# Kernel tuning notes

Measured on AMD Instinct MI355X. Metric: run time of the kernel, lower is better.

Reference implementation:

```python
import jax, jax.numpy as jnp
import numpy as np

STRIDES = [8, 16, 32]
INPUT = 640
NC = 80
NA = 3
B = 16
NGT = 32
LS = 0.0
BOX_W = 0.05 * 3.0
OBJ_W = 1.0 * 5.0
CLS_W = 0.5
NOOBJ_W = 0.5
IOU_THR = 0.5
EPS = 1e-7


def _bce(x, t):
    # BCEWithLogits, elementwise, numerically stable
    return jnp.maximum(x, 0.0) - x * t + jnp.log1p(jnp.exp(-jnp.abs(x)))


def _iou_gt_anchor(gt, anch):
    # gt: [..., 4] xyxy; anch: [..., 4] (cx, cy, w, h)
    ax1 = anch[..., 0] - anch[..., 2] * 0.5
    ay1 = anch[..., 1] - anch[..., 3] * 0.5
    ax2 = anch[..., 0] + anch[..., 2] * 0.5
    ay2 = anch[..., 1] + anch[..., 3] * 0.5
    iw = jnp.clip(jnp.minimum(gt[..., 2], ax2) - jnp.maximum(gt[..., 0], ax1), 0.0)
    ih = jnp.clip(jnp.minimum(gt[..., 3], ay2) - jnp.maximum(gt[..., 1], ay1), 0.0)
    inter = iw * ih
    a_gt = (gt[..., 2] - gt[..., 0]) * (gt[..., 3] - gt[..., 1])
    a_an = anch[..., 2] * anch[..., 3]
    return inter / (a_gt + a_an - inter + EPS)


def _assign_one(gt_boxes, gt_labels, anchors, stride):
    # Vectorized version of the per-box Python assignment loop.
    # gt_boxes: [N,4] xyxy; anchors: [A,H,W,4] cxcywh
    A, H, W, _ = anchors.shape
    N = gt_boxes.shape[0]
    gcx = (gt_boxes[:, 0] + gt_boxes[:, 2]) * 0.5
    gcy = (gt_boxes[:, 1] + gt_boxes[:, 3]) * 0.5
    gx = jnp.clip((gcx / stride).astype(jnp.int32), 0, W - 1)
    gy = jnp.clip((gcy / stride).astype(jnp.int32), 0, H - 1)
    cell = anchors[:, gy, gx, :]                      # [A, N, 4]
    iou = _iou_gt_anchor(gt_boxes[None, :, :], cell)  # [A, N]
    pos = iou > IOU_THR
    has = pos.any(axis=0)                             # [N]
    fb = jnp.arange(A)[:, None] == jnp.argmax(iou, axis=0)[None, :]
    pos = jnp.where(has[None, :], pos, fb)            # argmax fallback
    flat = gy * W + gx                                # [N]
    key = jnp.arange(A)[:, None] * (H * W) + flat[None, :]  # [A, N]
    cand = jnp.where(pos, iou, -1.0)
    best = jnp.full(A * H * W, -1.0, jnp.float32).at[key.ravel()].max(cand.ravel())
    gtid = jnp.broadcast_to(jnp.arange(N, dtype=jnp.int32)[None, :], (A, N))
    isb = pos & (cand >= best[key])
    win = jnp.full(A * H * W, N, jnp.int32).at[key.ravel()].min(
        jnp.where(isb, gtid, N).ravel().astype(jnp.int32))
    mask = win < N                                    # [A*H*W]
    wid = jnp.minimum(win, N - 1)
    obj_t = mask.astype(jnp.float32).reshape(A, H, W)
    oh = jax.nn.one_hot(gt_labels[wid], NC, dtype=jnp.float32)
    if LS > 0:
        oh = oh * (1.0 - LS) + LS / NC
    cls_t = (oh * mask[:, None].astype(jnp.float32)).reshape(A, H, W, NC)
    gt_cell = gt_boxes[wid].reshape(A, H, W, 4)
    return obj_t, cls_t, gt_cell


def _decode(box_pred, anchors, stride):
    # YOLOv5-style decode (assumed; _decode_boxes not in source snippet)
    s = jax.nn.sigmoid(box_pred)
    cx = anchors[..., 0] + (s[..., 0] * 2.0 - 0.5) * stride
    cy = anchors[..., 1] + (s[..., 1] * 2.0 - 0.5) * stride
    w = anchors[..., 2] * (s[..., 2] * 2.0) ** 2
    h = anchors[..., 3] * (s[..., 3] * 2.0) ** 2
    return jnp.stack([cx - w * 0.5, cy - h * 0.5, cx + w * 0.5, cy + h * 0.5], axis=-1)


def _ciou(b1, b2):
    # both xyxy, same shape; standard CIoU with detached alpha
    w1 = b1[..., 2] - b1[..., 0]; h1 = b1[..., 3] - b1[..., 1]
    w2 = b2[..., 2] - b2[..., 0]; h2 = b2[..., 3] - b2[..., 1]
    iw = jnp.clip(jnp.minimum(b1[..., 2], b2[..., 2]) - jnp.maximum(b1[..., 0], b2[..., 0]), 0.0)
    ih = jnp.clip(jnp.minimum(b1[..., 3], b2[..., 3]) - jnp.maximum(b1[..., 1], b2[..., 1]), 0.0)
    inter = iw * ih
    union = w1 * h1 + w2 * h2 - inter + EPS
    iou = inter / union
    cw = jnp.maximum(b1[..., 2], b2[..., 2]) - jnp.minimum(b1[..., 0], b2[..., 0])
    ch = jnp.maximum(b1[..., 3], b2[..., 3]) - jnp.minimum(b1[..., 1], b2[..., 1])
    c2 = cw ** 2 + ch ** 2 + EPS
    rho2 = ((b2[..., 0] + b2[..., 2] - b1[..., 0] - b1[..., 2]) ** 2 +
            (b2[..., 1] + b2[..., 3] - b1[..., 1] - b1[..., 3]) ** 2) * 0.25
    v = (4.0 / (jnp.pi ** 2)) * (jnp.arctan(w2 / (h2 + EPS)) - jnp.arctan(w1 / (h1 + EPS))) ** 2
    alpha = jax.lax.stop_gradient(v / (v - iou + (1.0 + EPS)))
    return iou - rho2 / c2 - alpha * v


def _scale_loss(pred, anch, gt_boxes, gt_labels, stride):
    box_pred = pred[..., :4]
    obj_pred = pred[..., 4]
    cls_pred = pred[..., 5:]
    obj_t, cls_t, gt_cell = jax.vmap(
        lambda b, l: _assign_one(b, l, anch, stride))(gt_boxes, gt_labels)
    pred_boxes = _decode(box_pred, anch, stride)           # [B,A,H,W,4]
    ciou = _ciou(pred_boxes, gt_cell)                       # [B,A,H,W]
    pos = obj_t > 0
    valid = pos & jnp.isfinite(ciou)
    n_valid = valid.sum()
    box_loss = jnp.where(valid, 1.0 - ciou, 0.0).sum() / jnp.maximum(n_valid, 1)
    wgt = jnp.where(pos, 1.0, NOOBJ_W)
    obj_loss = (_bce(obj_pred, obj_t) * wgt).sum() / (wgt.sum() + 1e-6)
    n_pos = pos.sum()
    cls_loss = (_bce(cls_pred, cls_t) * obj_t[..., None]).sum() / jnp.maximum(n_pos * NC, 1)
    return box_loss, obj_loss, cls_loss, n_valid


def _total(p0, p1, p2, a0, a1, a2, gt_boxes, gt_labels):
    bl = ol = cl = jnp.float32(0.0)
    tv = jnp.int32(0)
    for pred, anch, s in zip((p0, p1, p2), (a0, a1, a2), STRIDES):
        b, o, c, nv = _scale_loss(pred, anch, gt_boxes, gt_labels, float(s))
        bl = bl + b; ol = ol + o; cl = cl + c; tv = tv + nv
    ns = 3.0
    bl = jnp.where(tv > 0, bl / ns, bl)
    cl = jnp.where(tv > 0, cl / ns, cl)
    ol = ol / ns
    total = BOX_W * bl + OBJ_W * ol + CLS_W * cl
    return jnp.where(jnp.isfinite(total), total, 0.0)


def _make_anchors():
    wh = np.array([[[10, 13], [16, 30], [33, 23]],
                   [[30, 61], [62, 45], [59, 119]],
                   [[116, 90], [156, 198], [373, 326]]], np.float32)
    out = []
    for si, s in enumerate(STRIDES):
        H = W = INPUT // s
        yy, xx = np.meshgrid(np.arange(H), np.arange(W), indexing='ij')
        a = np.zeros((NA, H, W, 4), np.float32)
        a[..., 0] = ((xx + 0.5) * s).astype(np.float32)
        a[..., 1] = ((yy + 0.5) * s).astype(np.float32)
        a[..., 2] = wh[si, :, 0][:, None, None]
        a[..., 3] = wh[si, :, 1][:, None, None]
        out.append(jnp.asarray(a))
    return out


def setup_inputs() -> dict:
    key = jax.random.key(0)
    ks = jax.random.split(key, 6)
    p0 = jax.random.normal(ks[0], (B, NA, 80, 80, 5 + NC), jnp.float32)
    p1 = jax.random.normal(ks[1], (B, NA, 40, 40, 5 + NC), jnp.float32)
    p2 = jax.random.normal(ks[2], (B, NA, 20, 20, 5 + NC), jnp.float32)
    a0, a1, a2 = _make_anchors()
    cxy = jax.random.uniform(ks[3], (B, NGT, 2), jnp.float32, 32.0, INPUT - 32.0)
    wh = jax.random.uniform(ks[4], (B, NGT, 2), jnp.float32, 16.0, 256.0)
    x1y1 = jnp.clip(cxy - wh * 0.5, 0.0, float(INPUT))
    x2y2 = jnp.clip(cxy + wh * 0.5, 0.0, float(INPUT))
    gt_boxes = jnp.concatenate([x1y1, x2y2], axis=-1)
    gt_labels = jax.random.randint(ks[5], (B, NGT), 0, NC, jnp.int32)
    return {"p0": p0, "p1": p1, "p2": p2, "a0": a0, "a1": a1, "a2": a2,
            "gt_boxes": gt_boxes, "gt_labels": gt_labels}


def reference(p0, p1, p2, a0, a1, a2, gt_boxes, gt_labels):
    return _total(p0, p1, p2, a0, a1, a2, gt_boxes, gt_labels)
```

## Files before the change

kernel.cpp:

```cpp
#include <hip/hip_runtime.h>
#include <math.h>

#define NC 80
#define NA 3
#define BATCH 16
#define NGT 32
#define IOU_THR 0.5f
#define FEPS 1e-7f

#define ASSIGN_GRID 48
#define OBJ_BLOCKS 168
#define POS_BLOCKS 288
#define LOSS_GRID (OBJ_BLOCKS + POS_BLOCKS)

#define A_SLOT(a)  (128 * (a))
#define OBJ_SLOT(j) (6144 + 32 * (j))
#define POS_SLOT(j) (11520 + 32 * (j))

__device__ __forceinline__ float bce_f(float x, float t) {
    return fmaxf(x, 0.f) - x * t + log1pf(expf(-fabsf(x)));
}

__global__ __launch_bounds__(128) void assign_kernel(
    const float* __restrict__ gt_boxes,
    const float* __restrict__ a0, const float* __restrict__ a1, const float* __restrict__ a2,
    int* ws_i)
{
    const int bid = blockIdx.x;
    const int si = bid % 3;
    const int b  = bid / 3;
    const int W  = 80 >> si;
    const int HW = W * W;
    const float s = (float)(8 << si);
    const float* anch = (si == 0) ? a0 : (si == 1) ? a1 : a2;

    __shared__ float gtb[NGT][4];
    __shared__ int   gflat[NGT];
    __shared__ float giou[NA][NGT];
    __shared__ float gcand[NA][NGT];
    __shared__ unsigned char gpos[NA][NGT];
    __shared__ unsigned char gisb[NA][NGT];
    __shared__ int wlist[NA * NGT];
    __shared__ int wcnt2[2];
    __shared__ int s_wn;

    const int t = threadIdx.x;
    const int lane = t & 63, wv = t >> 6;
    gtb[t >> 2][t & 3] = gt_boxes[b * NGT * 4 + t];
    __syncthreads();

    if (t < NGT) {
        float x1 = gtb[t][0], y1 = gtb[t][1], x2 = gtb[t][2], y2 = gtb[t][3];
        float gcx = (x1 + x2) * 0.5f, gcy = (y1 + y2) * 0.5f;
        int gx = (int)(gcx / s); gx = min(max(gx, 0), W - 1);
        int gy = (int)(gcy / s); gy = min(max(gy, 0), W - 1);
        gflat[t] = gy * W + gx;
    }
    __syncthreads();

    if (t < NA * NGT) {
        int a = t >> 5, n = t & 31;
        int flat = gflat[n];
        const float* ap = anch + ((size_t)a * HW + flat) * 4;
        float acx = ap[0], acy = ap[1], aw = ap[2], ah = ap[3];
        float ax1 = acx - aw * 0.5f, ay1 = acy - ah * 0.5f;
        float ax2 = acx + aw * 0.5f, ay2 = acy + ah * 0.5f;
        float x1 = gtb[n][0], y1 = gtb[n][1], x2 = gtb[n][2], y2 = gtb[n][3];
        float iw = fmaxf(fminf(x2, ax2) - fmaxf(x1, ax1), 0.f);
        float ih = fmaxf(fminf(y2, ay2) - fmaxf(y1, ay1), 0.f);
        float inter = iw * ih;
        float a_gt = (x2 - x1) * (y2 - y1);
        float a_an = aw * ah;
        giou[a][n] = inter / (a_gt + a_an - inter + FEPS);
    }
    __syncthreads();

    if (t < NA * NGT) {
        int a = t >> 5, n = t & 31;
        float i0 = giou[0][n], i1 = giou[1][n], i2 = giou[2][n];
        bool has = (i0 > IOU_THR) || (i1 > IOU_THR) || (i2 > IOU_THR);
        int amax = 0; float bv = i0;
        if (i1 > bv) { bv = i1; amax = 1; }
        if (i2 > bv) { bv = i2; amax = 2; }
        float iou = giou[a][n];
        bool ps = has ? (iou > IOU_THR) : (a == amax);
        gpos[a][n] = ps ? 1 : 0;
        gcand[a][n] = ps ? iou : -1.0f;
    }
    __syncthreads();

    if (t < NA * NGT) {
        int a = t >> 5, n = t & 31;
        int flat = gflat[n];
        float best = -1.0f;
        for (int m = 0; m < NGT; ++m)
            if (gflat[m] == flat) best = fmaxf(best, gcand[a][m]);
        gisb[a][n] = (gpos[a][n] && gcand[a][n] >= best) ? 1 : 0;
    }
    __syncthreads();

    int win = 0, pack = 0;
    if (t < NA * NGT) {
        int a = t >> 5, n = t & 31;
        if (gisb[a][n]) {
            int flat = gflat[n];
            bool first = true;
            for (int m = 0; m < n; ++m)
                if (gflat[m] == flat && gisb[a][m]) { first = false; break; }
            if (first) { win = 1; pack = flat | (a << 13) | (n << 19); }
        }
    }
    unsigned long long mask = __ballot(win);
    if (lane == 0) wcnt2[wv] = (int)__popcll(mask);
    __syncthreads();
    if (win) {
        int base = wv ? wcnt2[0] : 0;
        int idx = base + (int)__popcll(mask & ((1ull << lane) - 1ull));
        wlist[idx] = pack;
    }
    if (t == 0) s_wn = wcnt2[0] + wcnt2[1];
    __syncthreads();
    const int wn = s_wn;

    int* slot = ws_i + A_SLOT(bid);
    if (t == 0) slot[0] = wn;
    if (t < 96) slot[1 + t] = (t < wn) ? wlist[t] : 0;
}

__global__ __launch_bounds__(256) void loss_kernel(
    const float* __restrict__ p0, const float* __restrict__ p1, const float* __restrict__ p2,
    const float* __restrict__ a0, const float* __restrict__ a1, const float* __restrict__ a2,
    const float* __restrict__ gt_boxes, const int* __restrict__ gt_labels,
    float* ws_f, const int* ws_i)
{
    const int bid = blockIdx.x;
    const int t = threadIdx.x;
    const int lane = t & 63, wv = t >> 6;
    __shared__ float red[4][4];

    if (bid < OBJ_BLOCKS) {
        int si, blk_local; const float* p;
        if (bid < 128)      { si = 0; blk_local = bid;       p = p0; }
        else if (bid < 160) { si = 1; blk_local = bid - 128; p = p1; }
        else                { si = 2; blk_local = bid - 160; p = p2; }
        int base_e = blk_local * 2400;
        float acc = 0.f;
        #pragma unroll 2
        for (int i = t; i < 2400; i += 256) {
            float x = p[(size_t)(base_e + i) * (5 + NC) + 4];
            acc += 0.5f * bce_f(x, 0.f);
        }
        #pragma unroll
        for (int off = 32; off; off >>= 1) acc += __shfl_down(acc, off);
        if (lane == 0) red[0][wv] = acc;
        __syncthreads();
        if (t == 0)
            ws_f[OBJ_SLOT(bid)] = red[0][0] + red[0][1] + red[0][2] + red[0][3];
        return;
    }

    const int pbid = bid - OBJ_BLOCKS;
    const int g48 = pbid / 6;
    const int sub = pbid % 6;
    const int si = g48 % 3;
    const int b  = g48 / 3;
    const int W  = 80 >> si;
    const int HW = W * W;
    const float s = (float)(8 << si);
    const float* p    = (si == 0) ? p0 : (si == 1) ? p1 : p2;
    const float* anch = (si == 0) ? a0 : (si == 1) ? a1 : a2;
    const int* aslot = ws_i + A_SLOT(g48);
    const int wn = aslot[0];

    const int g16 = t >> 4, l16 = t & 15;
    const int cell = sub * 16 + g16;
    float v_box = 0.f, v_nv = 0.f, v_cls = 0.f, v_obj = 0.f;
    if (cell < wn) {
        int e = aslot[1 + cell];
        int flat = e & 0x1FFF;
        int a = (e >> 13) & 3;
        int n = (e >> 19) & 31;
        const float* pred = p + (size_t)((b * NA + a) * HW + flat) * (5 + NC);

        int label = gt_labels[b * NGT + n];
        float csum = 0.f;
        #pragma unroll
        for (int jj = 0; jj < 5; ++jj) {
            int c = l16 + 16 * jj;
            float x = pred[5 + c];
            csum += bce_f(x, (c == label) ? 1.f : 0.f);
        }
        #pragma unroll
        for (int m = 8; m; m >>= 1) csum += __shfl_xor(csum, m);

        const float* ap = anch + ((size_t)a * HW + flat) * 4;
        float acx = ap[0], acy = ap[1], aw = ap[2], ah = ap[3];
        float s0 = 1.f / (1.f + expf(-pred[0]));
        float s1 = 1.f / (1.f + expf(-pred[1]));
        float s2 = 1.f / (1.f + expf(-pred[2]));
        float s3 = 1.f / (1.f + expf(-pred[3]));
        float cx = acx + (s0 * 2.f - 0.5f) * s;
        float cy = acy + (s1 * 2.f - 0.5f) * s;
        float pw = aw * (s2 * 2.f) * (s2 * 2.f);
        float ph = ah * (s3 * 2.f) * (s3 * 2.f);
        float b1x1 = cx - pw * 0.5f, b1y1 = cy - ph * 0.5f;
        float b1x2 = cx + pw * 0.5f, b1y2 = cy + ph * 0.5f;
        const float* gb = gt_boxes + (size_t)(b * NGT + n) * 4;
        float b2x1 = gb[0], b2y1 = gb[1], b2x2 = gb[2], b2y2 = gb[3];

        float w1 = b1x2 - b1x1, h1 = b1y2 - b1y1;
        float w2 = b2x2 - b2x1, h2 = b2y2 - b2y1;
        float iw = fmaxf(fminf(b1x2, b2x2) - fmaxf(b1x1, b2x1), 0.f);
        float ih = fmaxf(fminf(b1y2, b2y2) - fmaxf(b1y1, b2y1), 0.f);
        float inter = iw * ih;
        float uni = w1 * h1 + w2 * h2 - inter + FEPS;
        float iou = inter / uni;
        float cw = fmaxf(b1x2, b2x2) - fminf(b1x1, b2x1);
        float ch = fmaxf(b1y2, b2y2) - fminf(b1y1, b2y1);
        float c2 = cw * cw + ch * ch + FEPS;
        float dx = b2x1 + b2x2 - b1x1 - b1x2;
        float dy = b2y1 + b2y2 - b1y1 - b1y2;
        float rho2 = (dx * dx + dy * dy) * 0.25f;
        const float PI = 3.14159265358979323846f;
        float dv = atanf(w2 / (h2 + FEPS)) - atanf(w1 / (h1 + FEPS));
        float v = (4.f / (PI * PI)) * dv * dv;
        float alpha = v / (v - iou + (1.f + FEPS));
        float ciou = iou - rho2 / c2 - alpha * v;

        if (l16 == 0) {
            if (isfinite(ciou)) { v_box = 1.f - ciou; v_nv = 1.f; }
            v_cls = csum;
            float ox = pred[4];
            v_obj = bce_f(ox, 1.f) - 0.5f * bce_f(ox, 0.f);
        }
    }

    #pragma unroll
    for (int off = 32; off; off >>= 1) {
        v_box += __shfl_down(v_box, off);
        v_nv  += __shfl_down(v_nv,  off);
        v_cls += __shfl_down(v_cls, off);
        v_obj += __shfl_down(v_obj, off);
    }
    if (lane == 0) { red[0][wv] = v_box; red[1][wv] = v_nv; red[2][wv] = v_cls; red[3][wv] = v_obj; }
    __syncthreads();
    if (t == 0) {
        float* slot = ws_f + POS_SLOT(pbid);
        slot[0] = red[0][0] + red[0][1] + red[0][2] + red[0][3];
        slot[1] = red[1][0] + red[1][1] + red[1][2] + red[1][3];
        slot[2] = red[2][0] + red[2][1] + red[2][2] + red[2][3];
        slot[3] = red[3][0] + red[3][1] + red[3][2] + red[3][3];
    }
}

__global__ __launch_bounds__(256) void final_kernel(const float* ws_f, const int* ws_i,
                                                    float* __restrict__ out)
{
    const int t = threadIdx.x;
    const int lane = t & 63, wv = t >> 6;
    __shared__ float sc[3][6];

    if (wv < 3) {
        const int s = wv;
        float box = 0.f, nv = 0.f, cls = 0.f, oc = 0.f, np = 0.f, ob = 0.f;
        const int ocnt  = (s == 0) ? 128 : (s == 1) ? 32 : 8;
        const int obase = (s == 0) ? 0   : (s == 1) ? 128 : 160;
        for (int i = lane; i < ocnt; i += 64) ob += ws_f[OBJ_SLOT(obase + i)];
        for (int i = lane; i < 96; i += 64) {
            int m = i / 6, sub = i % 6;
            const float* ps = ws_f + POS_SLOT((3 * m + s) * 6 + sub);
            box += ps[0]; nv += ps[1]; cls += ps[2]; oc += ps[3];
        }
        if (lane < 16) np = (float)ws_i[A_SLOT(lane * 3 + s)];
        #pragma unroll
        for (int off = 32; off; off >>= 1) {
            box += __shfl_down(box, off);
            nv  += __shfl_down(nv,  off);
            cls += __shfl_down(cls, off);
            oc  += __shfl_down(oc,  off);
            np  += __shfl_down(np,  off);
            ob  += __shfl_down(ob,  off);
        }
        if (lane == 0) {
            sc[s][0] = box; sc[s][1] = nv; sc[s][2] = cls;
            sc[s][3] = oc;  sc[s][4] = np; sc[s][5] = ob;
        }
    }
    __syncthreads();
    if (t == 0) {
        float bl = 0.f, ol = 0.f, cl = 0.f;
        int tv = 0;
        for (int s = 0; s < 3; ++s) {
            int Wd = 80 >> s;
            int total = BATCH * NA * Wd * Wd;
            float nv = sc[s][1], np = sc[s][4];
            bl += sc[s][0] / fmaxf(nv, 1.f);
            float wsum = np + 0.5f * ((float)total - np);
            ol += (sc[s][5] + sc[s][3]) / (wsum + 1e-6f);
            cl += sc[s][2] / fmaxf(np * (float)NC, 1.f);
            tv += (int)nv;
        }
        if (tv > 0) { bl /= 3.f; cl /= 3.f; }
        ol /= 3.f;
        float total = 0.15f * bl + 5.0f * ol + 0.5f * cl;
        out[0] = isfinite(total) ? total : 0.f;
    }
}

extern "C" void kernel_launch(void* const* d_in, const int* in_sizes, int n_in,
                              void* d_out, int out_size, void* d_ws, size_t ws_size,
                              hipStream_t stream) {
    const float* p0  = (const float*)d_in[0];
    const float* p1  = (const float*)d_in[1];
    const float* p2  = (const float*)d_in[2];
    const float* a0  = (const float*)d_in[3];
    const float* a1  = (const float*)d_in[4];
    const float* a2  = (const float*)d_in[5];
    const float* gtb = (const float*)d_in[6];
    const int*   gtl = (const int*)d_in[7];

    assign_kernel<<<ASSIGN_GRID, 128, 0, stream>>>(gtb, a0, a1, a2, (int*)d_ws);
    loss_kernel<<<LOSS_GRID, 256, 0, stream>>>(
        p0, p1, p2, a0, a1, a2, gtb, gtl, (float*)d_ws, (const int*)d_ws);
    final_kernel<<<1, 256, 0, stream>>>((const float*)d_ws, (const int*)d_ws, (float*)d_out);
}
```

Measured before the change: 26.26 us.

## Fuse anchor assignment into positive-loss blocks, removing the separate assign kernel

```diff
diff --git a/kernel.cpp b/kernel.cpp
--- a/kernel.cpp
+++ b/kernel.cpp
@@ -8,45 +8,71 @@
 #define IOU_THR 0.5f
 #define FEPS 1e-7f
 
-#define ASSIGN_GRID 48
 #define OBJ_BLOCKS 168
 #define POS_BLOCKS 288
 #define LOSS_GRID (OBJ_BLOCKS + POS_BLOCKS)
 
-#define A_SLOT(a)  (128 * (a))
-#define OBJ_SLOT(j) (6144 + 32 * (j))
-#define POS_SLOT(j) (11520 + 32 * (j))
+#define OBJ_SLOT(j) (32 * (j))
+#define POS_SLOT(j) (5376 + 32 * (j))
 
 __device__ __forceinline__ float bce_f(float x, float t) {
     return fmaxf(x, 0.f) - x * t + log1pf(expf(-fabsf(x)));
 }
 
-__global__ __launch_bounds__(128) void assign_kernel(
-    const float* __restrict__ gt_boxes,
+__global__ __launch_bounds__(256) void loss_kernel(
+    const float* __restrict__ p0, const float* __restrict__ p1, const float* __restrict__ p2,
     const float* __restrict__ a0, const float* __restrict__ a1, const float* __restrict__ a2,
-    int* ws_i)
+    const float* __restrict__ gt_boxes, const int* __restrict__ gt_labels,
+    float* ws_f)
 {
     const int bid = blockIdx.x;
-    const int si = bid % 3;
-    const int b  = bid / 3;
+    const int t = threadIdx.x;
+    const int lane = t & 63, wv = t >> 6;
+    __shared__ float red[4][4];
+
+    if (bid < OBJ_BLOCKS) {
+        int blk_local; const float* p;
+        if (bid < 128)      { blk_local = bid;       p = p0; }
+        else if (bid < 160) { blk_local = bid - 128; p = p1; }
+        else                { blk_local = bid - 160; p = p2; }
+        int base_e = blk_local * 2400;
+        float acc = 0.f;
+        #pragma unroll 2
+        for (int i = t; i < 2400; i += 256) {
+            float x = p[(size_t)(base_e + i) * (5 + NC) + 4];
+            acc += 0.5f * bce_f(x, 0.f);
+        }
+        #pragma unroll
+        for (int off = 32; off; off >>= 1) acc += __shfl_down(acc, off);
+        if (lane == 0) red[0][wv] = acc;
+        __syncthreads();
+        if (t == 0)
+            ws_f[OBJ_SLOT(bid)] = red[0][0] + red[0][1] + red[0][2] + red[0][3];
+        return;
+    }
+
+    const int pbid = bid - OBJ_BLOCKS;
+    const int g48 = pbid / 6;
+    const int sub = pbid % 6;
+    const int si = g48 % 3;
+    const int b  = g48 / 3;
     const int W  = 80 >> si;
     const int HW = W * W;
     const float s = (float)(8 << si);
+    const float* p    = (si == 0) ? p0 : (si == 1) ? p1 : p2;
     const float* anch = (si == 0) ? a0 : (si == 1) ? a1 : a2;
 
     __shared__ float gtb[NGT][4];
     __shared__ int   gflat[NGT];
     __shared__ float giou[NA][NGT];
     __shared__ float gcand[NA][NGT];
-    __shared__ unsigned char gpos[NA][NGT];
+    __shared__ unsigned char gposm[NA][NGT];
     __shared__ unsigned char gisb[NA][NGT];
     __shared__ int wlist[NA * NGT];
-    __shared__ int wcnt2[2];
+    __shared__ int wcnt[4];
     __shared__ int s_wn;
 
-    const int t = threadIdx.x;
-    const int lane = t & 63, wv = t >> 6;
-    gtb[t >> 2][t & 3] = gt_boxes[b * NGT * 4 + t];
+    if (t < 128) gtb[t >> 2][t & 3] = gt_boxes[b * NGT * 4 + t];
     __syncthreads();
 
     if (t < NGT) {
@@ -84,7 +110,7 @@
         if (i2 > bv) { bv = i2; amax = 2; }
         float iou = giou[a][n];
         bool ps = has ? (iou > IOU_THR) : (a == amax);
-        gpos[a][n] = ps ? 1 : 0;
+        gposm[a][n] = ps ? 1 : 0;
         gcand[a][n] = ps ? iou : -1.0f;
     }
     __syncthreads();
@@ -95,7 +121,7 @@
         float best = -1.0f;
         for (int m = 0; m < NGT; ++m)
             if (gflat[m] == flat) best = fmaxf(best, gcand[a][m]);
-        gisb[a][n] = (gpos[a][n] && gcand[a][n] >= best) ? 1 : 0;
+        gisb[a][n] = (gposm[a][n] && gcand[a][n] >= best) ? 1 : 0;
     }
     __syncthreads();
 
@@ -111,72 +137,23 @@
         }
     }
     unsigned long long mask = __ballot(win);
-    if (lane == 0) wcnt2[wv] = (int)__popcll(mask);
+    if (lane == 0) wcnt[wv] = (int)__popcll(mask);
     __syncthreads();
     if (win) {
-        int base = wv ? wcnt2[0] : 0;
+        int base = 0;
+        for (int w2 = 0; w2 < wv; ++w2) base += wcnt[w2];
         int idx = base + (int)__popcll(mask & ((1ull << lane) - 1ull));
         wlist[idx] = pack;
     }
-    if (t == 0) s_wn = wcnt2[0] + wcnt2[1];
+    if (t == 0) s_wn = wcnt[0] + wcnt[1] + wcnt[2] + wcnt[3];
     __syncthreads();
     const int wn = s_wn;
-
-    int* slot = ws_i + A_SLOT(bid);
-    if (t == 0) slot[0] = wn;
-    if (t < 96) slot[1 + t] = (t < wn) ? wlist[t] : 0;
-}
-
-__global__ __launch_bounds__(256) void loss_kernel(
-    const float* __restrict__ p0, const float* __restrict__ p1, const float* __restrict__ p2,
-    const float* __restrict__ a0, const float* __restrict__ a1, const float* __restrict__ a2,
-    const float* __restrict__ gt_boxes, const int* __restrict__ gt_labels,
-    float* ws_f, const int* ws_i)
-{
-    const int bid = blockIdx.x;
-    const int t = threadIdx.x;
-    const int lane = t & 63, wv = t >> 6;
-    __shared__ float red[4][4];
-
-    if (bid < OBJ_BLOCKS) {
-        int si, blk_local; const float* p;
-        if (bid < 128)      { si = 0; blk_local = bid;       p = p0; }
-        else if (bid < 160) { si = 1; blk_local = bid - 128; p = p1; }
-        else                { si = 2; blk_local = bid - 160; p = p2; }
-        int base_e = blk_local * 2400;
-        float acc = 0.f;
-        #pragma unroll 2
-        for (int i = t; i < 2400; i += 256) {
-            float x = p[(size_t)(base_e + i) * (5 + NC) + 4];
-            acc += 0.5f * bce_f(x, 0.f);
-        }
-        #pragma unroll
-        for (int off = 32; off; off >>= 1) acc += __shfl_down(acc, off);
-        if (lane == 0) red[0][wv] = acc;
-        __syncthreads();
-        if (t == 0)
-            ws_f[OBJ_SLOT(bid)] = red[0][0] + red[0][1] + red[0][2] + red[0][3];
-        return;
-    }
-
-    const int pbid = bid - OBJ_BLOCKS;
-    const int g48 = pbid / 6;
-    const int sub = pbid % 6;
-    const int si = g48 % 3;
-    const int b  = g48 / 3;
-    const int W  = 80 >> si;
-    const int HW = W * W;
-    const float s = (float)(8 << si);
-    const float* p    = (si == 0) ? p0 : (si == 1) ? p1 : p2;
-    const float* anch = (si == 0) ? a0 : (si == 1) ? a1 : a2;
-    const int* aslot = ws_i + A_SLOT(g48);
-    const int wn = aslot[0];
 
     const int g16 = t >> 4, l16 = t & 15;
     const int cell = sub * 16 + g16;
     float v_box = 0.f, v_nv = 0.f, v_cls = 0.f, v_obj = 0.f;
     if (cell < wn) {
-        int e = aslot[1 + cell];
+        int e = wlist[cell];
         int flat = e & 0x1FFF;
         int a = (e >> 13) & 3;
         int n = (e >> 19) & 31;
@@ -205,8 +182,8 @@
         float ph = ah * (s3 * 2.f) * (s3 * 2.f);
         float b1x1 = cx - pw * 0.5f, b1y1 = cy - ph * 0.5f;
         float b1x2 = cx + pw * 0.5f, b1y2 = cy + ph * 0.5f;
-        const float* gb = gt_boxes + (size_t)(b * NGT + n) * 4;
-        float b2x1 = gb[0], b2y1 = gb[1], b2x2 = gb[2], b2y2 = gb[3];
+        float b2x1 = gtb[n][0], b2y1 = gtb[n][1];
+        float b2x2 = gtb[n][2], b2y2 = gtb[n][3];
 
         float w1 = b1x2 - b1x1, h1 = b1y2 - b1y1;
         float w2 = b2x2 - b2x1, h2 = b2y2 - b2y1;
@@ -250,10 +227,11 @@
         slot[1] = red[1][0] + red[1][1] + red[1][2] + red[1][3];
         slot[2] = red[2][0] + red[2][1] + red[2][2] + red[2][3];
         slot[3] = red[3][0] + red[3][1] + red[3][2] + red[3][3];
+        slot[4] = (float)wn;
     }
 }
 
-__global__ __launch_bounds__(256) void final_kernel(const float* ws_f, const int* ws_i,
+__global__ __launch_bounds__(256) void final_kernel(const float* ws_f,
                                                     float* __restrict__ out)
 {
     const int t = threadIdx.x;
@@ -270,8 +248,8 @@
             int m = i / 6, sub = i % 6;
             const float* ps = ws_f + POS_SLOT((3 * m + s) * 6 + sub);
             box += ps[0]; nv += ps[1]; cls += ps[2]; oc += ps[3];
-        }
-        if (lane < 16) np = (float)ws_i[A_SLOT(lane * 3 + s)];
+            if (sub == 0) np += ps[4];
+        }
         #pragma unroll
         for (int off = 32; off; off >>= 1) {
             box += __shfl_down(box, off);
@@ -319,8 +297,7 @@
     const float* gtb = (const float*)d_in[6];
     const int*   gtl = (const int*)d_in[7];
 
-    assign_kernel<<<ASSIGN_GRID, 128, 0, stream>>>(gtb, a0, a1, a2, (int*)d_ws);
     loss_kernel<<<LOSS_GRID, 256, 0, stream>>>(
-        p0, p1, p2, a0, a1, a2, gtb, gtl, (float*)d_ws, (const int*)d_ws);
-    final_kernel<<<1, 256, 0, stream>>>((const float*)d_ws, (const int*)d_ws, (float*)d_out);
+        p0, p1, p2, a0, a1, a2, gtb, gtl, (float*)d_ws);
+    final_kernel<<<1, 256, 0, stream>>>((const float*)d_ws, (float*)d_out);
 }
```

After: 22.88 us (median of 2 runs). 1.15x faster.
